# Kernel optimization log

Hardware: AMD Instinct MI355X
Metric: run time of the kernel (lower is better)

The kernel has to match this reference:

```python
import jax, jax.numpy as jnp
import numpy as np

TAU = 2.0
V_TH = 1.0
SG_ALPHA = 4.0  # spikingjelly sigmoid surrogate default

@jax.custom_vjp
def spike_fn(x):
    # Heaviside forward, sigmoid surrogate backward
    return (x >= 0.0).astype(x.dtype)

def _spike_fwd(x):
    return spike_fn(x), x

def _spike_bwd(x, g):
    s = jax.nn.sigmoid(SG_ALPHA * x)
    return (g * SG_ALPHA * s * (1.0 - s),)

spike_fn.defvjp(_spike_fwd, _spike_bwd)


def setup_inputs() -> dict:
    key = jax.random.key(0)
    k1, k2, k3 = jax.random.split(key, 3)
    T, B, D, K = 1024, 16, 512, 31
    inputs = jax.random.normal(k1, (T, B, D), dtype=jnp.float32)
    w_pw = jax.random.normal(k2, (D, D), dtype=jnp.float32) * (1.0 / np.sqrt(D))
    b_pw = jnp.zeros((D,), dtype=jnp.float32)
    w_dw = jax.random.normal(k3, (D, K), dtype=jnp.float32) * (1.0 / np.sqrt(K))
    return {"inputs": inputs, "w_pw": w_pw, "b_pw": b_pw, "w_dw": w_dw}


def reference(inputs, w_pw, b_pw, w_dw):
    # inputs: (T, B, D)
    T, B, D = inputs.shape
    K = w_dw.shape[1]
    pad = (K - 1) // 2
    # trans1: (T,B,D) -> (B,D,T)
    x = jnp.transpose(inputs, (1, 2, 0))
    # pointwise conv1d (1x1): channel mixing
    x = jnp.einsum('bdt,ed->bet', x, w_pw) + b_pw[None, :, None]
    # depthwise conv1d, same padding, no bias
    x = jax.lax.conv_general_dilated(
        x, w_dw[:, None, :], window_strides=(1,), padding=[(pad, pad)],
        feature_group_count=D, dimension_numbers=('NCH', 'OIH', 'NCH'))
    # trans2: (B,D,T) -> (T,B,D)
    x = jnp.transpose(x, (2, 0, 1))

    # multi-step LIF: decay_input=False, v_reset=0 -> v = v*(1-1/tau) + x
    decay = 1.0 - 1.0 / TAU

    def step(v, x_t):
        v = v * decay + x_t
        s = spike_fn(v - V_TH)
        # hard reset with detach_reset=True
        v = v * (1.0 - jax.lax.stop_gradient(s))
        return v, s

    v0 = jnp.zeros((B, D), dtype=inputs.dtype)
    _, spikes = jax.lax.scan(step, v0, x)
    return spikes + inputs
```

## Files before the change

### kernel.cpp

```cpp
#include <hip/hip_runtime.h>

#define T_DIM 1024
#define B_DIM 16
#define D_DIM 512
#define K_W   31
#define PAD   15
#define ST    (B_DIM * D_DIM)


#define S_E 146
#define S_T 130
__global__ __launch_bounds__(256, 2)
void pw_gemm(const float* __restrict__ inp, const float* __restrict__ w_pw,
             const float* __restrict__ b_pw, float* __restrict__ Yw,
             int tau0, int tau1, int NTW)
{
#pragma clang fp contract(off)
    __shared__ float Es[2][32 * S_E];
    __shared__ float Ts[2][32 * S_T];

    const int tid = threadIdx.x;
    const int e0  = blockIdx.x * 128;
    int tg0 = tau0 + blockIdx.y * 128;
    if (tg0 + 128 > tau1) {
        int s = tau1 - 128;
        tg0 = (s > tau0) ? s : tau0;
    }
    const int b  = blockIdx.z;
    const int rt = tid >> 4;
    const int ce = tid & 15;
    const int eoff = ce * 8 + ((ce >> 2) << 2);

    float acc[8][8];
#pragma unroll
    for (int i = 0; i < 8; ++i)
#pragma unroll
        for (int j = 0; j < 8; ++j) acc[i][j] = 0.0f;

    float4 av[4], xv[4];

#pragma unroll
    for (int i = 0; i < 4; ++i) {
        int cid = tid + 256 * i;
        int row = cid >> 3;
        int kq  = cid & 7;
        int trow = tg0 + row;
        if (trow > T_DIM - 1) trow = T_DIM - 1;
        av[i] = *(const float4*)&w_pw[(size_t)(e0 + row) * D_DIM + kq * 4];
        xv[i] = *(const float4*)&inp[(size_t)trow * (B_DIM * D_DIM)
                                     + (size_t)b * D_DIM + kq * 4];
    }
#pragma unroll
    for (int i = 0; i < 4; ++i) {
        int cid = tid + 256 * i;
        int row = cid >> 3;
        int kq  = cid & 7;
        int srow = row + ((row >> 5) << 2);
        Es[0][(kq * 4 + 0) * S_E + srow] = av[i].x;
        Es[0][(kq * 4 + 1) * S_E + srow] = av[i].y;
        Es[0][(kq * 4 + 2) * S_E + srow] = av[i].z;
        Es[0][(kq * 4 + 3) * S_E + srow] = av[i].w;
        Ts[0][(kq * 4 + 0) * S_T + row] = xv[i].x;
        Ts[0][(kq * 4 + 1) * S_T + row] = xv[i].y;
        Ts[0][(kq * 4 + 2) * S_T + row] = xv[i].z;
        Ts[0][(kq * 4 + 3) * S_T + row] = xv[i].w;
    }

    int cur = 0;
    for (int k0 = 0; k0 < D_DIM; k0 += 32) {
        __syncthreads();

        const bool has_next = (k0 + 32 < D_DIM);
        if (has_next) {
#pragma unroll
            for (int i = 0; i < 4; ++i) {
                int cid = tid + 256 * i;
                int row = cid >> 3;
                int kq  = cid & 7;
                int trow = tg0 + row;
                if (trow > T_DIM - 1) trow = T_DIM - 1;
                av[i] = *(const float4*)&w_pw[(size_t)(e0 + row) * D_DIM
                                              + k0 + 32 + kq * 4];
                xv[i] = *(const float4*)&inp[(size_t)trow * (B_DIM * D_DIM)
                                             + (size_t)b * D_DIM + k0 + 32 + kq * 4];
            }
        }

#pragma unroll 8
        for (int kk = 0; kk < 32; ++kk) {
            float4 tf0 = *(const float4*)&Ts[cur][kk * S_T + rt * 8];
            float4 tf1 = *(const float4*)&Ts[cur][kk * S_T + rt * 8 + 4];
            float4 ef0 = *(const float4*)&Es[cur][kk * S_E + eoff];
            float4 ef1 = *(const float4*)&Es[cur][kk * S_E + eoff + 4];
            float a[8] = {tf0.x, tf0.y, tf0.z, tf0.w, tf1.x, tf1.y, tf1.z, tf1.w};
            float x[8] = {ef0.x, ef0.y, ef0.z, ef0.w, ef1.x, ef1.y, ef1.z, ef1.w};
#pragma unroll
            for (int i = 0; i < 8; ++i)
#pragma unroll
                for (int j = 0; j < 8; ++j)
                    acc[i][j] = __fadd_rn(acc[i][j], __fmul_rn(a[i], x[j]));
        }

        if (has_next) {
            const int nxt = cur ^ 1;
#pragma unroll
            for (int i = 0; i < 4; ++i) {
                int cid = tid + 256 * i;
                int row = cid >> 3;
                int kq  = cid & 7;
                int srow = row + ((row >> 5) << 2);
                Es[nxt][(kq * 4 + 0) * S_E + srow] = av[i].x;
                Es[nxt][(kq * 4 + 1) * S_E + srow] = av[i].y;
                Es[nxt][(kq * 4 + 2) * S_E + srow] = av[i].z;
                Es[nxt][(kq * 4 + 3) * S_E + srow] = av[i].w;
                Ts[nxt][(kq * 4 + 0) * S_T + row] = xv[i].x;
                Ts[nxt][(kq * 4 + 1) * S_T + row] = xv[i].y;
                Ts[nxt][(kq * 4 + 2) * S_T + row] = xv[i].z;
                Ts[nxt][(kq * 4 + 3) * S_T + row] = xv[i].w;
            }
            cur = nxt;
        }
    }

    float bias[8];
#pragma unroll
    for (int j = 0; j < 8; ++j) bias[j] = b_pw[e0 + ce * 8 + j];

#pragma unroll
    for (int i = 0; i < 8; ++i) {
        int tau = tg0 + rt * 8 + i;
        if (tau < tau1) {
            float* yrow = Yw + ((size_t)b * NTW + (tau - tau0)) * D_DIM + e0 + ce * 8;
#pragma unroll
            for (int j = 0; j < 8; ++j)
                yrow[j] = __fadd_rn(acc[i][j], bias[j]);
        }
    }
}

__global__ __launch_bounds__(64, 2)
void dwlif(const float* __restrict__ Yw, const float* __restrict__ w_dw,
           const float* __restrict__ inp, float* __restrict__ out,
           int t0p, int tau0, int NTW)
{
#pragma clang fp contract(off)
    const int lane  = threadIdx.x;
    const int d     = blockIdx.x * 64 + lane;
    const int chunk = blockIdx.y;
    const int b     = blockIdx.z;

    const int cstart = t0p + 128 * chunk;
    int ts = cstart - 64; if (ts < 0) ts = 0;
    const int ngroups = (cstart == 0) ? 16 : 24;
    const int outg    = ngroups - 16;

    float wd[K_W];
#pragma unroll
    for (int k = 0; k < K_W; ++k) wd[k] = w_dw[d * K_W + k];

    const float* __restrict__ ybase = Yw  + (size_t)b * NTW * D_DIM + d;
    const float* __restrict__ xbase = inp + (size_t)b * D_DIM + d;
    float*       __restrict__ obase = out + (size_t)b * D_DIM + d;

    auto YLD = [&](int tau) -> float {
        int idx = tau - tau0;
        idx = idx < 0 ? 0 : idx;
        idx = idx >= NTW ? NTW - 1 : idx;
        float ld = ybase[(size_t)idx * D_DIM];
        return (tau >= 0 && tau < T_DIM) ? ld : 0.0f;
    };

    float yw[54], pf0[8], pf1[8], xq0[8], xq1[8];
#pragma unroll
    for (int i = 0; i < 54; ++i) yw[i] = YLD(ts - PAD + i);
#pragma unroll
    for (int j = 0; j < 8; ++j) pf0[j] = YLD(ts + 39 + j);
    if (outg == 0) {
#pragma unroll
        for (int j = 0; j < 8; ++j) xq0[j] = xbase[(size_t)(ts + j) * ST];
    }

    float v = 0.0f;

#define GROUP(G_EXPR, PF_IN, PF_OUT, XQ_IN, XQ_OUT)                          \
    {                                                                        \
        const int g  = (G_EXPR);                                             \
        const int tg = ts + 8 * g;                                           \
        _Pragma("unroll")                                                    \
        for (int j = 0; j < 8; ++j) PF_OUT[j] = YLD(tg + 47 + j);            \
        if (g + 1 >= outg) {                            \
            _Pragma("unroll")                                                \
            for (int j = 0; j < 8; ++j) {                                    \
                int tx = tg + 8 + j;                                         \
                tx = (tx > T_DIM - 1) ? T_DIM - 1 : tx;      \
                XQ_OUT[j] = xbase[(size_t)tx * ST];                          \
            }                                                                \
        }                                                                    \
        _Pragma("unroll")                                                    \
        for (int s = 0; s < 8; ++s) {                                        \
            float z = 0.0f;                                                  \
            _Pragma("unroll")                                                \
            for (int k = 0; k < K_W; ++k)            \
                z = __fadd_rn(z, __fmul_rn(wd[k], yw[s + k]));               \
            v = __fadd_rn(__fmul_rn(v, 0.5f), z);                            \
            const bool sp = (v >= 1.0f);                                     \
            if (g >= outg)                                                   \
                obase[(size_t)(tg + s) * ST] =                               \
                    __fadd_rn(sp ? 1.0f : 0.0f, XQ_IN[s]);                   \
            v = sp ? 0.0f : v;                      \
        }                                                                    \
        _Pragma("unroll")                                                    \
        for (int i = 0; i < 46; ++i) yw[i] = yw[i + 8];                      \
        _Pragma("unroll")                                                    \
        for (int j = 0; j < 8; ++j) yw[46 + j] = PF_IN[j];                   \
    }

    for (int it = 0; it < ngroups; it += 2) {
        GROUP(it,     pf0, pf1, xq0, xq1);
        GROUP(it + 1, pf1, pf0, xq1, xq0);
    }
#undef GROUP
}

extern "C" void kernel_launch(void* const* d_in, const int* in_sizes, int n_in,
                              void* d_out, int out_size, void* d_ws, size_t ws_size,
                              hipStream_t stream)
{
    const float* inp  = (const float*)d_in[0];
    const float* w_pw = (const float*)d_in[1];
    const float* b_pw = (const float*)d_in[2];
    const float* w_dw = (const float*)d_in[3];
    float* out = (float*)d_out;

    auto need = [](int L) -> size_t {
        int ntw = (L + 94 > T_DIM) ? T_DIM : (L + 94);
        return (size_t)ntw * (ST * sizeof(float));
    };
    int L = 128;
    if      (ws_size >= need(1024)) L = 1024;
    else if (ws_size >= need(512))  L = 512;
    else if (ws_size >= need(256))  L = 256;

    const int NTWmax = (L + 94 > T_DIM) ? T_DIM : (L + 94);
    float* Yw = (float*)d_ws;
    (void)NTWmax;

    const int P = T_DIM / L;
    for (int p = 0; p < P; ++p) {
        const int t0   = p * L;
        const int t1   = t0 + L;
        const int tau0 = (t0 - 79 > 0) ? (t0 - 79) : 0;
        const int tau1 = (t1 + PAD < T_DIM) ? (t1 + PAD) : T_DIM;
        const int NTW  = tau1 - tau0;

        dim3 g1(D_DIM / 128, (NTW + 127) / 128, B_DIM);
        pw_gemm<<<g1, 256, 0, stream>>>(inp, w_pw, b_pw, Yw, tau0, tau1, NTW);

        dim3 g2(D_DIM / 64, L / 128, B_DIM);
        dwlif<<<g2, 64, 0, stream>>>(Yw, w_dw, inp, out, t0, tau0, NTW);
    }
}
```

Baseline: 152.8 us.

## Split GEMM shared-memory tiles into half-k buffers to raise occupancy

The pointwise GEMM's double-buffered 32-wide k tiles in shared memory become two 16-wide half buffers, cutting LDS per block roughly in half, and launch bounds go from 2 to 3 blocks. Global loads for the next 32-wide tile are kept in registers and written to shared memory in half-tile pieces, alternating with compute on the other half. The aim is more resident blocks to hide memory latency. The cost is four barriers per 32-k step instead of one, and extra register-held prefetch buffers that could pressure the tighter register budget.

```diff
diff --git a/kernel.cpp b/kernel.cpp
--- a/kernel.cpp
+++ b/kernel.cpp
@@ -10,14 +10,14 @@
 
 #define S_E 146
 #define S_T 130
-__global__ __launch_bounds__(256, 2)
+__global__ __launch_bounds__(256, 3)
 void pw_gemm(const float* __restrict__ inp, const float* __restrict__ w_pw,
              const float* __restrict__ b_pw, float* __restrict__ Yw,
              int tau0, int tau1, int NTW)
 {
 #pragma clang fp contract(off)
-    __shared__ float Es[2][32 * S_E];
-    __shared__ float Ts[2][32 * S_T];
+    __shared__ float EsH[2][16 * S_E];
+    __shared__ float TsH[2][16 * S_T];
 
     const int tid = threadIdx.x;
     const int e0  = blockIdx.x * 128;
@@ -37,90 +37,83 @@
 #pragma unroll
         for (int j = 0; j < 8; ++j) acc[i][j] = 0.0f;
 
-    float4 av[4], xv[4];
-
-#pragma unroll
-    for (int i = 0; i < 4; ++i) {
-        int cid = tid + 256 * i;
-        int row = cid >> 3;
-        int kq  = cid & 7;
-        int trow = tg0 + row;
-        if (trow > T_DIM - 1) trow = T_DIM - 1;
-        av[i] = *(const float4*)&w_pw[(size_t)(e0 + row) * D_DIM + kq * 4];
-        xv[i] = *(const float4*)&inp[(size_t)trow * (B_DIM * D_DIM)
-                                     + (size_t)b * D_DIM + kq * 4];
-    }
-#pragma unroll
-    for (int i = 0; i < 4; ++i) {
-        int cid = tid + 256 * i;
-        int row = cid >> 3;
-        int kq  = cid & 7;
-        int srow = row + ((row >> 5) << 2);
-        Es[0][(kq * 4 + 0) * S_E + srow] = av[i].x;
-        Es[0][(kq * 4 + 1) * S_E + srow] = av[i].y;
-        Es[0][(kq * 4 + 2) * S_E + srow] = av[i].z;
-        Es[0][(kq * 4 + 3) * S_E + srow] = av[i].w;
-        Ts[0][(kq * 4 + 0) * S_T + row] = xv[i].x;
-        Ts[0][(kq * 4 + 1) * S_T + row] = xv[i].y;
-        Ts[0][(kq * 4 + 2) * S_T + row] = xv[i].z;
-        Ts[0][(kq * 4 + 3) * S_T + row] = xv[i].w;
-    }
-
-    int cur = 0;
-    for (int k0 = 0; k0 < D_DIM; k0 += 32) {
-        __syncthreads();
-
-        const bool has_next = (k0 + 32 < D_DIM);
-        if (has_next) {
-#pragma unroll
-            for (int i = 0; i < 4; ++i) {
-                int cid = tid + 256 * i;
-                int row = cid >> 3;
-                int kq  = cid & 7;
-                int trow = tg0 + row;
-                if (trow > T_DIM - 1) trow = T_DIM - 1;
-                av[i] = *(const float4*)&w_pw[(size_t)(e0 + row) * D_DIM
-                                              + k0 + 32 + kq * 4];
-                xv[i] = *(const float4*)&inp[(size_t)trow * (B_DIM * D_DIM)
-                                             + (size_t)b * D_DIM + k0 + 32 + kq * 4];
-            }
-        }
-
-#pragma unroll 8
-        for (int kk = 0; kk < 32; ++kk) {
-            float4 tf0 = *(const float4*)&Ts[cur][kk * S_T + rt * 8];
-            float4 tf1 = *(const float4*)&Ts[cur][kk * S_T + rt * 8 + 4];
-            float4 ef0 = *(const float4*)&Es[cur][kk * S_E + eoff];
-            float4 ef1 = *(const float4*)&Es[cur][kk * S_E + eoff + 4];
-            float a[8] = {tf0.x, tf0.y, tf0.z, tf0.w, tf1.x, tf1.y, tf1.z, tf1.w};
-            float x[8] = {ef0.x, ef0.y, ef0.z, ef0.w, ef1.x, ef1.y, ef1.z, ef1.w};
-#pragma unroll
-            for (int i = 0; i < 8; ++i)
-#pragma unroll
-                for (int j = 0; j < 8; ++j)
-                    acc[i][j] = __fadd_rn(acc[i][j], __fmul_rn(a[i], x[j]));
-        }
-
-        if (has_next) {
-            const int nxt = cur ^ 1;
-#pragma unroll
-            for (int i = 0; i < 4; ++i) {
-                int cid = tid + 256 * i;
-                int row = cid >> 3;
-                int kq  = cid & 7;
-                int srow = row + ((row >> 5) << 2);
-                Es[nxt][(kq * 4 + 0) * S_E + srow] = av[i].x;
-                Es[nxt][(kq * 4 + 1) * S_E + srow] = av[i].y;
-                Es[nxt][(kq * 4 + 2) * S_E + srow] = av[i].z;
-                Es[nxt][(kq * 4 + 3) * S_E + srow] = av[i].w;
-                Ts[nxt][(kq * 4 + 0) * S_T + row] = xv[i].x;
-                Ts[nxt][(kq * 4 + 1) * S_T + row] = xv[i].y;
-                Ts[nxt][(kq * 4 + 2) * S_T + row] = xv[i].z;
-                Ts[nxt][(kq * 4 + 3) * S_T + row] = xv[i].w;
-            }
-            cur = nxt;
-        }
-    }
+    float4 avE[4], xvE[4], avO[4], xvO[4];
+
+#define LOADT(AV, XV, T)                                                     \
+    {                                                                        \
+        const int kbase = (T) * 32;                                          \
+        _Pragma("unroll")                                                    \
+        for (int i = 0; i < 4; ++i) {                                        \
+            int cid = tid + 256 * i;                                         \
+            int row = cid >> 3;                                              \
+            int kq  = tid & 7;                                               \
+            int trow = tg0 + row;                                            \
+            if (trow > T_DIM - 1) trow = T_DIM - 1;                          \
+            AV[i] = *(const float4*)&w_pw[(size_t)(e0 + row) * D_DIM         \
+                                          + kbase + kq * 4];                 \
+            XV[i] = *(const float4*)&inp[(size_t)trow * ST                   \
+                                         + (size_t)b * D_DIM + kbase + kq * 4]; \
+        }                                                                    \
+    }
+
+#define WRH(AV, XV, H)                                                       \
+    if (((tid >> 2) & 1) == (H)) {                                           \
+        _Pragma("unroll")                                                    \
+        for (int i = 0; i < 4; ++i) {                                        \
+            int cid = tid + 256 * i;                                         \
+            int row = cid >> 3;                                              \
+            int kq2 = tid & 3;                                               \
+            int srow = row + ((row >> 5) << 2);                 \
+            EsH[H][(kq2 * 4 + 0) * S_E + srow] = AV[i].x;                    \
+            EsH[H][(kq2 * 4 + 1) * S_E + srow] = AV[i].y;                    \
+            EsH[H][(kq2 * 4 + 2) * S_E + srow] = AV[i].z;                    \
+            EsH[H][(kq2 * 4 + 3) * S_E + srow] = AV[i].w;                    \
+            TsH[H][(kq2 * 4 + 0) * S_T + row] = XV[i].x;                     \
+            TsH[H][(kq2 * 4 + 1) * S_T + row] = XV[i].y;                     \
+            TsH[H][(kq2 * 4 + 2) * S_T + row] = XV[i].z;                     \
+            TsH[H][(kq2 * 4 + 3) * S_T + row] = XV[i].w;                     \
+        }                                                                    \
+    }
+
+#define CMP(H)                                                               \
+    _Pragma("unroll 8")                                                      \
+    for (int kk = 0; kk < 16; ++kk) {                                        \
+        float4 tf0 = *(const float4*)&TsH[H][kk * S_T + rt * 8];             \
+        float4 tf1 = *(const float4*)&TsH[H][kk * S_T + rt * 8 + 4];         \
+        float4 ef0 = *(const float4*)&EsH[H][kk * S_E + eoff];               \
+        float4 ef1 = *(const float4*)&EsH[H][kk * S_E + eoff + 4];           \
+        float a[8] = {tf0.x, tf0.y, tf0.z, tf0.w, tf1.x, tf1.y, tf1.z, tf1.w}; \
+        float x[8] = {ef0.x, ef0.y, ef0.z, ef0.w, ef1.x, ef1.y, ef1.z, ef1.w}; \
+        _Pragma("unroll")                                                    \
+        for (int i = 0; i < 8; ++i)                                          \
+            _Pragma("unroll")                                                \
+            for (int j = 0; j < 8; ++j)                                      \
+                acc[i][j] = __fadd_rn(acc[i][j], __fmul_rn(a[i], x[j]));     \
+    }
+
+    LOADT(avE, xvE, 0);
+    WRH(avE, xvE, 0);
+
+    for (int it = 0; it < 16; it += 2) {
+        __syncthreads();
+        LOADT(avO, xvO, it + 1);
+        CMP(0);
+        WRH(avE, xvE, 1);
+        __syncthreads();
+        CMP(1);
+        WRH(avO, xvO, 0);
+
+        __syncthreads();
+        if (it + 2 < 16) LOADT(avE, xvE, it + 2);
+        CMP(0);
+        WRH(avO, xvO, 1);
+        __syncthreads();
+        CMP(1);
+        if (it + 2 < 16) WRH(avE, xvE, 0);
+    }
+#undef LOADT
+#undef WRH
+#undef CMP
 
     float bias[8];
 #pragma unroll
@@ -241,9 +234,7 @@
     else if (ws_size >= need(512))  L = 512;
     else if (ws_size >= need(256))  L = 256;
 
-    const int NTWmax = (L + 94 > T_DIM) ? T_DIM : (L + 94);
     float* Yw = (float*)d_ws;
-    (void)NTWmax;
 
     const int P = T_DIM / L;
     for (int p = 0; p < P; ++p) {
```

After: 247.8 us. 1.62x slower.
